# Optimization experiments

Hardware: AMD Instinct MI355X
Metric: run time of the kernel (lower is better)

Reference implementation:

```python
import jax, jax.numpy as jnp
import numpy as np

N = 100000   # nodes per node type
E = 1000000  # edges per edge type
C = 128      # channels
H = 4        # num_heads
D = C // H   # head_dim


def setup_inputs() -> dict:
    key = jax.random.key(0)
    ks = jax.random.split(key, 16)
    return {
        "x_A": jax.random.normal(ks[0], (N, C), jnp.float32),
        "x_B": jax.random.normal(ks[1], (N, C), jnp.float32),
        "Wq": jax.random.normal(ks[2], (C, C), jnp.float32) * 0.05,
        "bq": jax.random.normal(ks[3], (C,), jnp.float32) * 0.05,
        "Wk": jax.random.normal(ks[4], (C, C), jnp.float32) * 0.05,
        "bk": jax.random.normal(ks[5], (C,), jnp.float32) * 0.05,
        "Wv": jax.random.normal(ks[6], (C, C), jnp.float32) * 0.05,
        "bv": jax.random.normal(ks[7], (C,), jnp.float32) * 0.05,
        "gamma": jnp.ones((C,), jnp.float32),
        "beta": jnp.zeros((C,), jnp.float32),
        "bias_AB": jax.random.normal(ks[8], (1,), jnp.float32),
        "bias_BA": jax.random.normal(ks[9], (1,), jnp.float32),
        "sb_AB": jax.random.normal(ks[10], (E,), jnp.float32),
        "sb_BA": jax.random.normal(ks[11], (E,), jnp.float32),
        "edge_index_AB": jax.random.randint(ks[12], (2, E), 0, N, jnp.int32),
        "edge_index_BA": jax.random.randint(ks[13], (2, E), 0, N, jnp.int32),
    }


def _edge_attention(x_src, x_dst, src, dst, sb, etype_bias, Wq, bq, Wk, bk, Wv, bv):
    """Per-edge-type attention: gather -> score -> dst-segment softmax -> scatter-add."""
    n_dst = x_dst.shape[0]
    Q = (x_dst @ Wq.T + bq).reshape(n_dst, H, D)
    K = (x_src @ Wk.T + bk).reshape(-1, H, D)
    V = (x_src @ Wv.T + bv).reshape(-1, H, D)
    # [E, H] per-edge scores
    scores = jnp.einsum('ehd,ehd->eh', Q[dst], K[src]) / np.float32(np.sqrt(D))
    scores = scores + sb[:, None] + etype_bias  # spatial bias + edge-type bias
    # segment softmax over edges grouped by dst node (numerically stable)
    m = jax.ops.segment_max(scores, dst, num_segments=n_dst)
    ex = jnp.exp(scores - m[dst])
    denom = jax.ops.segment_sum(ex, dst, num_segments=n_dst)
    w = ex / denom[dst]  # [E, H]
    msg = (V[src] * w[:, :, None]).reshape(-1, C)  # [E, C]
    return jax.ops.segment_sum(msg, dst, num_segments=n_dst)  # index_add_


def _layernorm(x, gamma, beta, eps=1e-5):
    mu = x.mean(-1, keepdims=True)
    var = ((x - mu) ** 2).mean(-1, keepdims=True)
    return (x - mu) / jnp.sqrt(var + eps) * gamma + beta


def _forward(x_A, x_B, Wq, bq, Wk, bk, Wv, bv, gamma, beta,
             bias_AB, bias_BA, sb_AB, sb_BA, edge_index_AB, edge_index_BA):
    src_ab, dst_ab = edge_index_AB[0], edge_index_AB[1]  # A -> B
    src_ba, dst_ba = edge_index_BA[0], edge_index_BA[1]  # B -> A
    lin = (Wq, bq, Wk, bk, Wv, bv)
    out_B = _edge_attention(x_A, x_B, src_ab, dst_ab, sb_AB, bias_AB, *lin)
    out_A = _edge_attention(x_B, x_A, src_ba, dst_ba, sb_BA, bias_BA, *lin)
    # total degree = in_deg + out_deg per node type
    ones_e = jnp.ones((E,), jnp.float32)
    deg_A = (jax.ops.segment_sum(ones_e, src_ab, num_segments=N)
             + jax.ops.segment_sum(ones_e, dst_ba, num_segments=N))
    deg_B = (jax.ops.segment_sum(ones_e, dst_ab, num_segments=N)
             + jax.ops.segment_sum(ones_e, src_ba, num_segments=N))
    out_A = out_A + deg_A[:, None]
    out_B = out_B + deg_B[:, None]
    out_A = _layernorm(out_A + x_A, gamma, beta)
    out_B = _layernorm(out_B + x_B, gamma, beta)
    return out_A, out_B


def reference(x_A, x_B, Wq, bq, Wk, bk, Wv, bv, gamma, beta,
              bias_AB, bias_BA, sb_AB, sb_BA, edge_index_AB, edge_index_BA):
    return _forward(x_A, x_B, Wq, bq, Wk, bk, Wv, bv, gamma, beta,
                    bias_AB, bias_BA, sb_AB, sb_BA, edge_index_AB, edge_index_BA)
```

## Files before the change

### kernel.cpp

```cpp
#include <hip/hip_runtime.h>

#define CH 128
#define QSCALE (0.17677669529663687f * 1.4426950408889634f)
#define LOG2E 1.4426950408889634f
#define SCAN_BLK 1024
#define KVSTRIDE 384

typedef _Float16 f16;
typedef _Float16 f16x2 __attribute__((ext_vector_type(2)));
typedef _Float16 f16x8 __attribute__((ext_vector_type(8)));
typedef __attribute__((ext_vector_type(4))) float f32x4;

__device__ __forceinline__ unsigned pk2(float a, float b) {
    auto h = __builtin_amdgcn_cvt_pkrtz(a, b);
    return __builtin_bit_cast(unsigned, h);
}
__device__ __forceinline__ f16x2 u2h(unsigned u) { return __builtin_bit_cast(f16x2, u); }

template <int CTRL>
__device__ __forceinline__ float dpp_add(float x) {
    const int t = __builtin_amdgcn_update_dpp(0, __builtin_bit_cast(int, x), CTRL, 0xF, 0xF, false);
    return x + __builtin_bit_cast(float, t);
}
__device__ __forceinline__ float head_sum(float x) {
    x = dpp_add<0xB1>(x);
    x = dpp_add<0x4E>(x);
    x = dpp_add<0x124>(x);
    x = dpp_add<0x128>(x);
    return x;
}

__global__ __launch_bounds__(256) void wcvt(const float* __restrict__ Wq, const float* __restrict__ Wk,
                                            const float* __restrict__ Wv, unsigned short* __restrict__ out)
{
    const int i = blockIdx.x * 256 + threadIdx.x;
    if (i >= 3 * CH * CH) return;
    const float* W = (i < CH * CH) ? Wq : (i < 2 * CH * CH) ? Wk : Wv;
    const float s = (i < CH * CH) ? QSCALE : 1.f;
    f16 h = (f16)(W[i & (CH * CH - 1)] * s);
    out[i] = __builtin_bit_cast(unsigned short, h);
}

__global__ __launch_bounds__(256) void qkv_mfma(
    const float* __restrict__ xA, const float* __restrict__ xB,
    const unsigned short* __restrict__ Wb,
    const float* __restrict__ bq, const float* __restrict__ bk, const float* __restrict__ bv,
    unsigned short* __restrict__ Qb,
    unsigned char* __restrict__ KVb,
    int n)
{
    __shared__ __align__(16) char lds[40960];
    const int type = blockIdx.y;
    const float* x = type ? xB : xA;
    const int bRow = blockIdx.x * 64;
    const int tid = threadIdx.x;

    #pragma unroll
    for (int j = 0; j < 8; ++j) {
        const int flat16 = j * 256 + tid;
        const int row = flat16 >> 5;
        const int c16 = flat16 & 31;
        float4 v = make_float4(0.f, 0.f, 0.f, 0.f);
        if (bRow + row < n) v = *(const float4*)(x + (size_t)(bRow + row) * CH + c16 * 4);
        const int off = (row * 256 + c16 * 8) ^ ((row & 7) << 4);
        *(uint2*)(lds + off) = make_uint2(pk2(v.x, v.y), pk2(v.z, v.w));
    }
    __syncthreads();

    const int w = tid >> 6, l = tid & 63, lr = l & 15, lg = l >> 4;
    const int colbase = w * 32;

    f32x4 acc[3][2][4];
    #pragma unroll
    for (int p = 0; p < 3; ++p)
        #pragma unroll
        for (int ct = 0; ct < 2; ++ct)
            #pragma unroll
            for (int rt = 0; rt < 4; ++rt)
                acc[p][ct][rt] = (f32x4){0.f, 0.f, 0.f, 0.f};

    #pragma unroll
    for (int kt = 0; kt < 4; ++kt) {
        f16x8 bx[4];
        #pragma unroll
        for (int rt = 0; rt < 4; ++rt) {
            const int row = rt * 16 + lr;
            const int off = (row * 256 + kt * 64 + lg * 16) ^ ((row & 7) << 4);
            bx[rt] = *(const f16x8*)(lds + off);
        }
        #pragma unroll
        for (int p = 0; p < 3; ++p) {
            #pragma unroll
            for (int ct = 0; ct < 2; ++ct) {
                const int ocol = colbase + ct * 16 + lr;
                const f16x8 a = *(const f16x8*)(Wb + ((size_t)p << 14) + (size_t)ocol * CH + kt * 32 + lg * 8);
                #pragma unroll
                for (int rt = 0; rt < 4; ++rt)
                    acc[p][ct][rt] = __builtin_amdgcn_mfma_f32_16x16x32_f16(a, bx[rt], acc[p][ct][rt], 0, 0, 0);
            }
        }
    }

    __syncthreads();

    #pragma unroll
    for (int ct = 0; ct < 2; ++ct) {
        const int c0 = colbase + ct * 16 + lg * 4;
        float4 bbq = *(const float4*)(bq + c0);
        bbq.x *= QSCALE; bbq.y *= QSCALE; bbq.z *= QSCALE; bbq.w *= QSCALE;
        const float4 bbk = *(const float4*)(bk + c0);
        const float4 bbv = *(const float4*)(bv + c0);
        const int cbq = w * 64 + ct * 32 + lg * 8;
        const int cbk = w * 32 + ct * 16 + lg * 4;
        #pragma unroll
        for (int rt = 0; rt < 4; ++rt) {
            const int nl = rt * 16 + lr;
            const int swz = (nl & 7) << 4;
            const f32x4 aq = acc[0][ct][rt], ak = acc[1][ct][rt], av = acc[2][ct][rt];
            *(uint2*)(lds + nl * 256 + (cbq ^ swz)) =
                make_uint2(pk2(aq[0] + bbq.x, aq[1] + bbq.y), pk2(aq[2] + bbq.z, aq[3] + bbq.w));
            int kw = __builtin_amdgcn_cvt_pk_fp8_f32(ak[0] + bbk.x, ak[1] + bbk.y, 0, false);
            kw     = __builtin_amdgcn_cvt_pk_fp8_f32(ak[2] + bbk.z, ak[3] + bbk.w, kw, true);
            *(unsigned*)(lds + 16384 + nl * 128 + (cbk ^ swz)) = (unsigned)kw;
            *(uint2*)(lds + 24576 + nl * 256 + (cbq ^ swz)) =
                make_uint2(pk2(av[0] + bbv.x, av[1] + bbv.y), pk2(av[2] + bbv.z, av[3] + bbv.w));
        }
    }
    __syncthreads();

    unsigned short* Qo = Qb + (size_t)type * n * CH;
    unsigned char* KVo = KVb + (size_t)type * n * KVSTRIDE;
    #pragma unroll
    for (int j = 0; j < 4; ++j) {
        const int flat = j * 256 + tid;
        const int row = flat >> 4, c16 = flat & 15;
        const uint4 val = *(const uint4*)(lds + row * 256 + ((c16 ^ (row & 7)) << 4));
        const int node = bRow + row;
        if (node < n) *(uint4*)(Qo + (size_t)node * CH + c16 * 8) = val;
    }
    #pragma unroll
    for (int j = 0; j < 2; ++j) {
        const int flat = j * 256 + tid;
        const int row = flat >> 3, c = flat & 7;
        const uint4 val = *(const uint4*)(lds + 16384 + row * 128 + ((c ^ (row & 7)) << 4));
        const int node = bRow + row;
        if (node < n) *(uint4*)(KVo + (size_t)node * KVSTRIDE + c * 16) = val;
    }
    #pragma unroll
    for (int j = 0; j < 4; ++j) {
        const int flat = j * 256 + tid;
        const int row = flat >> 4, c16 = flat & 15;
        const uint4 val = *(const uint4*)(lds + 24576 + row * 256 + ((c16 ^ (row & 7)) << 4));
        const int node = bRow + row;
        if (node < n) *(uint4*)(KVo + (size_t)node * KVSTRIDE + 128 + c16 * 16) = val;
    }
}

__global__ __launch_bounds__(256) void deg_hist(const int* __restrict__ eiAB, const int* __restrict__ eiBA,
                                                int* __restrict__ degAB, int* __restrict__ degBA,
                                                int nE, int ebl)
{
    const int dir = blockIdx.x >= ebl;
    const int e = ((blockIdx.x - dir * ebl) * 256 + threadIdx.x) * 4;
    if (e >= nE) return;
    const int* ei = dir ? eiBA : eiAB;
    int* deg = dir ? degBA : degAB;
    if (e + 3 < nE) {
        const int4 d4 = *(const int4*)(ei + nE + e);
        atomicAdd(&deg[d4.x], 1); atomicAdd(&deg[d4.y], 1);
        atomicAdd(&deg[d4.z], 1); atomicAdd(&deg[d4.w], 1);
    } else {
        for (int j = e; j < nE; ++j) atomicAdd(&deg[ei[nE + j]], 1);
    }
}

__global__ __launch_bounds__(256) void scan_local(const int* __restrict__ degAB, const int* __restrict__ degBA,
                                                  int* __restrict__ offsAB, int* __restrict__ offsBA,
                                                  int* __restrict__ bsums, int n, int nb)
{
    __shared__ int s[256];
    const int dir = blockIdx.x >= nb;
    const int blk = blockIdx.x - dir * nb;
    const int* deg = dir ? degBA : degAB;
    int* offs = dir ? offsBA : offsAB;
    int* bs = bsums + dir * 256;

    const int t = threadIdx.x;
    const int base = blk * SCAN_BLK + t * 4;
    int v0 = 0, v1 = 0, v2 = 0, v3 = 0;
    if (base + 3 < n) {
        int4 q = *(const int4*)(deg + base);
        v0 = q.x; v1 = q.y; v2 = q.z; v3 = q.w;
    } else {
        if (base + 0 < n) v0 = deg[base + 0];
        if (base + 1 < n) v1 = deg[base + 1];
        if (base + 2 < n) v2 = deg[base + 2];
    }
    const int tsum = v0 + v1 + v2 + v3;
    s[t] = tsum;
    __syncthreads();
    for (int off = 1; off < 256; off <<= 1) {
        int add = (t >= off) ? s[t - off] : 0;
        __syncthreads();
        s[t] += add;
        __syncthreads();
    }
    const int excl = s[t] - tsum;
    if (base + 0 < n) offs[base + 0] = excl;
    if (base + 1 < n) offs[base + 1] = excl + v0;
    if (base + 2 < n) offs[base + 2] = excl + v0 + v1;
    if (base + 3 < n) offs[base + 3] = excl + v0 + v1 + v2;
    if (t == 255) bs[blk] = s[255];
}

__global__ __launch_bounds__(256) void scan_bsums(int* __restrict__ bsums, int nb)
{
    __shared__ int s[256];
    int* bs = bsums + blockIdx.x * 256;
    const int t = threadIdx.x;
    int v = (t < nb) ? bs[t] : 0;
    s[t] = v;
    __syncthreads();
    for (int off = 1; off < 256; off <<= 1) {
        int add = (t >= off) ? s[t - off] : 0;
        __syncthreads();
        s[t] += add;
        __syncthreads();
    }
    if (t < nb) bs[t] = s[t] - v;
}

__global__ __launch_bounds__(256) void add_bsums(int* __restrict__ offsAB, int* __restrict__ offsBA,
                                                 int* __restrict__ curAB, int* __restrict__ curBA,
                                                 const int* __restrict__ bsums, int n, int nbl)
{
    const int dir = blockIdx.x >= nbl;
    const int i = (blockIdx.x - dir * nbl) * 256 + threadIdx.x;
    if (i >= n) return;
    int* offs = dir ? offsBA : offsAB;
    int* cur  = dir ? curBA  : curAB;
    const int v = offs[i] + bsums[dir * 256 + (i >> 10)];
    offs[i] = v;
    cur[i] = v;
}

__global__ __launch_bounds__(256) void csr_fill(const int* __restrict__ eiAB, const int* __restrict__ eiBA,
                                                const float* __restrict__ sbAB, const float* __restrict__ sbBA,
                                                const float* __restrict__ biasAB, const float* __restrict__ biasBA,
                                                int* __restrict__ curAB, int* __restrict__ curBA,
                                                int2* __restrict__ edAB, int2* __restrict__ edBA,
                                                int nE, int ebl)
{
    const int dir = blockIdx.x >= ebl;
    const int e = ((blockIdx.x - dir * ebl) * 256 + threadIdx.x) * 4;
    if (e >= nE) return;
    const int* ei = dir ? eiBA : eiAB;
    const float* sb = dir ? sbBA : sbAB;
    const float bia = dir ? biasBA[0] : biasAB[0];
    int* cur = dir ? curBA : curAB;
    int2* ed = dir ? edBA : edAB;
    if (e + 3 < nE) {
        const int4 s4 = *(const int4*)(ei + e);
        const int4 d4 = *(const int4*)(ei + nE + e);
        const float4 b4 = *(const float4*)(sb + e);
        int p0 = atomicAdd(&cur[d4.x], 1); ed[p0] = make_int2(s4.x, __float_as_int((b4.x + bia) * LOG2E));
        int p1 = atomicAdd(&cur[d4.y], 1); ed[p1] = make_int2(s4.y, __float_as_int((b4.y + bia) * LOG2E));
        int p2 = atomicAdd(&cur[d4.z], 1); ed[p2] = make_int2(s4.z, __float_as_int((b4.z + bia) * LOG2E));
        int p3 = atomicAdd(&cur[d4.w], 1); ed[p3] = make_int2(s4.w, __float_as_int((b4.w + bia) * LOG2E));
    } else {
        for (int j = e; j < nE; ++j) {
            const int pos = atomicAdd(&cur[ei[nE + j]], 1);
            ed[pos] = make_int2(ei[j], __float_as_int((sb[j] + bia) * LOG2E));
        }
    }
}

__global__ __launch_bounds__(256) void attn_node(
    const unsigned short* __restrict__ Qb,
    const unsigned char* __restrict__ KVb,
    const float* __restrict__ xA, const float* __restrict__ xB,
    const int* __restrict__ offsAB, const int* __restrict__ offsBA,
    const int* __restrict__ degAB, const int* __restrict__ degBA,
    const int2* __restrict__ edAB, const int2* __restrict__ edBA,
    const float* __restrict__ gamma, const float* __restrict__ beta,
    float* __restrict__ out, int n, int abl)
{
    const int dir = blockIdx.x >= abl;
    const int node = (blockIdx.x - dir * abl) * 4 + (threadIdx.x >> 6);
    if (node >= n) return;
    const int l = threadIdx.x & 63;
    const int l2 = l * 2;

    const unsigned short* Q = Qb + (size_t)dir * n * CH;
    const unsigned char* KV = KVb + (size_t)(1 - dir) * n * KVSTRIDE;
    const float* x = dir ? xB : xA;
    const int* offs = dir ? offsAB : offsBA;
    const int* deg  = dir ? degAB  : degBA;
    const int2* ed  = dir ? edAB   : edBA;
    float* o = out + (size_t)dir * n * CH;

    const f16x2 qp = u2h(*(const unsigned*)(Q + (size_t)node * CH + l2));
    const float qf0 = (float)qp[0], qf1 = (float)qp[1];

    const int beg = __builtin_amdgcn_readfirstlane(offs[node]);
    const int d   = __builtin_amdgcn_readfirstlane(deg[node]);

    float m = -3.0e38f, den = 0.f;
    f16x2 a01 = (f16x2){(f16)0.f, (f16)0.f};

    auto loadE = [&](int i, float& sbf, unsigned& kc, unsigned& vc) {
        if (i < d) {
            const int2 e = ed[beg + i];
            sbf = __int_as_float(e.y);
            const unsigned b = (unsigned)e.x * (unsigned)KVSTRIDE;
            kc = *(const unsigned short*)(KV + b + l2);
            vc = *(const unsigned*)(KV + b + 128 + l2 * 2);
        } else {
            sbf = __int_as_float((int)0xFF800000u);
            kc = 0; vc = 0;
        }
    };

    auto procPair = [&](float sf0, unsigned k0, unsigned v0,
                        float sf1, unsigned k1, unsigned v1) {
        const auto kf0 = __builtin_amdgcn_cvt_pk_f32_fp8((int)k0, false);
        const auto kf1 = __builtin_amdgcn_cvt_pk_f32_fp8((int)k1, false);
        float sa = head_sum(fmaf(qf0, kf0[0], qf1 * kf0[1])) + sf0;
        float sb = head_sum(fmaf(qf0, kf1[0], qf1 * kf1[1])) + sf1;
        const float pm = fmaxf(sa, sb);
        if (!__all(pm <= m + 8.f)) {
            const float mn = fmaxf(m, pm);
            const float sc = exp2f(m - mn);
            den *= sc;
            a01 *= u2h(pk2(sc, sc));
            m = mn;
        }
        const float ea = exp2f(sa - m);
        const float eb = exp2f(sb - m);
        den += ea + eb;
        a01 += u2h(pk2(ea, ea)) * u2h(v0);
        a01 += u2h(pk2(eb, eb)) * u2h(v1);
    };

    float sA0, sA1, sA2, sA3, sB0, sB1, sB2, sB3;
    unsigned kA0, kA1, kA2, kA3, kB0, kB1, kB2, kB3;
    unsigned vA0, vA1, vA2, vA3, vB0, vB1, vB2, vB3;
    loadE(0, sA0, kA0, vA0); loadE(1, sA1, kA1, vA1);
    loadE(2, sA2, kA2, vA2); loadE(3, sA3, kA3, vA3);
    loadE(4, sB0, kB0, vB0); loadE(5, sB1, kB1, vB1);
    loadE(6, sB2, kB2, vB2); loadE(7, sB3, kB3, vB3);

    for (int i = 0; i < d; i += 8) {
        procPair(sA0, kA0, vA0, sA1, kA1, vA1);
        procPair(sA2, kA2, vA2, sA3, kA3, vA3);
        loadE(i + 8,  sA0, kA0, vA0); loadE(i + 9,  sA1, kA1, vA1);
        loadE(i + 10, sA2, kA2, vA2); loadE(i + 11, sA3, kA3, vA3);
        procPair(sB0, kB0, vB0, sB1, kB1, vB1);
        procPair(sB2, kB2, vB2, sB3, kB3, vB3);
        loadE(i + 12, sB0, kB0, vB0); loadE(i + 13, sB1, kB1, vB1);
        loadE(i + 14, sB2, kB2, vB2); loadE(i + 15, sB3, kB3, vB3);
    }

    const float inv = (den > 0.f) ? 1.f / den : 0.f;
    const float2 xv = *(const float2*)(x + (size_t)node * CH + l2);
    const float w0 = (float)a01[0] * inv + xv.x;
    const float w1 = (float)a01[1] * inv + xv.y;

    float sum = w0 + w1;
    #pragma unroll
    for (int off = 32; off; off >>= 1) sum += __shfl_xor(sum, off);
    const float mean = sum * (1.f / 128.f);
    const float c0 = w0 - mean, c1 = w1 - mean;
    float vs = c0 * c0 + c1 * c1;
    #pragma unroll
    for (int off = 32; off; off >>= 1) vs += __shfl_xor(vs, off);
    const float rstd = rsqrtf(vs * (1.f / 128.f) + 1e-5f);

    const float2 g = *(const float2*)(gamma + l2);
    const float2 bt = *(const float2*)(beta + l2);
    float2 ov;
    ov.x = c0 * rstd * g.x + bt.x;
    ov.y = c1 * rstd * g.y + bt.y;
    *(float2*)(o + (size_t)node * CH + l2) = ov;
}

extern "C" void kernel_launch(void* const* d_in, const int* in_sizes, int n_in,
                              void* d_out, int out_size, void* d_ws, size_t ws_size,
                              hipStream_t stream)
{
    const float* xA     = (const float*)d_in[0];
    const float* xB     = (const float*)d_in[1];
    const float* Wq     = (const float*)d_in[2];
    const float* bq     = (const float*)d_in[3];
    const float* Wk     = (const float*)d_in[4];
    const float* bk     = (const float*)d_in[5];
    const float* Wv     = (const float*)d_in[6];
    const float* bv     = (const float*)d_in[7];
    const float* gamma  = (const float*)d_in[8];
    const float* beta   = (const float*)d_in[9];
    const float* biasAB = (const float*)d_in[10];
    const float* biasBA = (const float*)d_in[11];
    const float* sbAB   = (const float*)d_in[12];
    const float* sbBA   = (const float*)d_in[13];
    const int*   eiAB   = (const int*)d_in[14];
    const int*   eiBA   = (const int*)d_in[15];

    const int n  = in_sizes[0] / CH;
    const int nE = in_sizes[12];
    const size_t NC = (size_t)n * CH;

    char* p = (char*)d_ws;
    auto carve = [&](size_t bytes) { char* r = p; p += (bytes + 15) & ~(size_t)15; return r; };
    unsigned short* Qb = (unsigned short*)carve(2 * NC * 2);
    unsigned char*  KVb = (unsigned char*)carve((size_t)2 * n * KVSTRIDE);
    unsigned short* Wb  = (unsigned short*)carve(3 * CH * CH * 2);
    int2* edAB  = (int2*)carve((size_t)nE * 8);
    int2* edBA  = (int2*)carve((size_t)nE * 8);
    int* offsAB = (int*)carve((size_t)n * 4);
    int* offsBA = (int*)carve((size_t)n * 4);
    int* degAB  = (int*)carve((size_t)2 * n * 4);
    int* degBA  = degAB + n;
    int* curAB  = (int*)carve((size_t)n * 4);
    int* curBA  = (int*)carve((size_t)n * 4);
    int* bsums  = (int*)carve(2 * 256 * 4);

    float* out = (float*)d_out;

    (void)hipMemsetAsync(degAB, 0, (size_t)2 * n * sizeof(int), stream);

    wcvt<<<(3 * CH * CH + 255) / 256, 256, 0, stream>>>(Wq, Wk, Wv, Wb);

    dim3 qkv_grid((n + 63) / 64, 2);
    qkv_mfma<<<qkv_grid, 256, 0, stream>>>(xA, xB, Wb, bq, bk, bv, Qb, KVb, n);

    const int ebl4 = (nE + 1023) / 1024;
    deg_hist<<<2 * ebl4, 256, 0, stream>>>(eiAB, eiBA, degAB, degBA, nE, ebl4);

    const int nb = (n + SCAN_BLK - 1) / SCAN_BLK;
    scan_local<<<2 * nb, 256, 0, stream>>>(degAB, degBA, offsAB, offsBA, bsums, n, nb);
    scan_bsums<<<2, 256, 0, stream>>>(bsums, nb);
    const int nbl = (n + 255) / 256;
    add_bsums<<<2 * nbl, 256, 0, stream>>>(offsAB, offsBA, curAB, curBA, bsums, n, nbl);

    csr_fill<<<2 * ebl4, 256, 0, stream>>>(eiAB, eiBA, sbAB, sbBA, biasAB, biasBA,
                                           curAB, curBA, edAB, edBA, nE, ebl4);

    const int abl = (n + 3) / 4;
    attn_node<<<2 * abl, 256, 0, stream>>>(Qb, KVb, xA, xB, offsAB, offsBA, degAB, degBA,
                                           edAB, edBA, gamma, beta, out, n, abl);
}
```

Baseline: 488.7 us.

## Process two nodes per wavefront with 4 channels per lane in attention

The attention kernel now maps each half-wave (32 lanes) to one destination node, so each lane handles 4 channels instead of 2. Per-head score reduction drops to three DPP steps and the LayerNorm shuffles shrink to 5 rounds. The CSR fill pre-multiplies source indices by the KV row stride to save a multiply per edge. The loop runs to the max degree of the two paired nodes, so work is wasted when their degrees differ, and edge loads are clamped instead of predicated.

```diff
diff --git a/kernel.cpp b/kernel.cpp
--- a/kernel.cpp
+++ b/kernel.cpp
@@ -22,11 +22,10 @@
     const int t = __builtin_amdgcn_update_dpp(0, __builtin_bit_cast(int, x), CTRL, 0xF, 0xF, false);
     return x + __builtin_bit_cast(float, t);
 }
-__device__ __forceinline__ float head_sum(float x) {
+__device__ __forceinline__ float head_sum8(float x) {
     x = dpp_add<0xB1>(x);
     x = dpp_add<0x4E>(x);
-    x = dpp_add<0x124>(x);
-    x = dpp_add<0x128>(x);
+    x = dpp_add<0x141>(x);
     return x;
 }
 
@@ -263,14 +262,14 @@
         const int4 s4 = *(const int4*)(ei + e);
         const int4 d4 = *(const int4*)(ei + nE + e);
         const float4 b4 = *(const float4*)(sb + e);
-        int p0 = atomicAdd(&cur[d4.x], 1); ed[p0] = make_int2(s4.x, __float_as_int((b4.x + bia) * LOG2E));
-        int p1 = atomicAdd(&cur[d4.y], 1); ed[p1] = make_int2(s4.y, __float_as_int((b4.y + bia) * LOG2E));
-        int p2 = atomicAdd(&cur[d4.z], 1); ed[p2] = make_int2(s4.z, __float_as_int((b4.z + bia) * LOG2E));
-        int p3 = atomicAdd(&cur[d4.w], 1); ed[p3] = make_int2(s4.w, __float_as_int((b4.w + bia) * LOG2E));
+        int p0 = atomicAdd(&cur[d4.x], 1); ed[p0] = make_int2(s4.x * KVSTRIDE, __float_as_int((b4.x + bia) * LOG2E));
+        int p1 = atomicAdd(&cur[d4.y], 1); ed[p1] = make_int2(s4.y * KVSTRIDE, __float_as_int((b4.y + bia) * LOG2E));
+        int p2 = atomicAdd(&cur[d4.z], 1); ed[p2] = make_int2(s4.z * KVSTRIDE, __float_as_int((b4.z + bia) * LOG2E));
+        int p3 = atomicAdd(&cur[d4.w], 1); ed[p3] = make_int2(s4.w * KVSTRIDE, __float_as_int((b4.w + bia) * LOG2E));
     } else {
         for (int j = e; j < nE; ++j) {
             const int pos = atomicAdd(&cur[ei[nE + j]], 1);
-            ed[pos] = make_int2(ei[j], __float_as_int((sb[j] + bia) * LOG2E));
+            ed[pos] = make_int2(ei[j] * KVSTRIDE, __float_as_int((sb[j] + bia) * LOG2E));
         }
     }
 }
@@ -286,10 +285,12 @@
     float* __restrict__ out, int n, int abl)
 {
     const int dir = blockIdx.x >= abl;
-    const int node = (blockIdx.x - dir * abl) * 4 + (threadIdx.x >> 6);
-    if (node >= n) return;
     const int l = threadIdx.x & 63;
-    const int l2 = l * 2;
+    const int w = threadIdx.x >> 6;
+    const int half = l >> 5;
+    const int h = l & 31;
+    const int node = (blockIdx.x - dir * abl) * 8 + w * 2 + half;
+    const int nodec = min(node, n - 1);
 
     const unsigned short* Q = Qb + (size_t)dir * n * CH;
     const unsigned char* KV = KVb + (size_t)(1 - dir) * n * KVSTRIDE;
@@ -299,89 +300,95 @@
     const int2* ed  = dir ? edAB   : edBA;
     float* o = out + (size_t)dir * n * CH;
 
-    const f16x2 qp = u2h(*(const unsigned*)(Q + (size_t)node * CH + l2));
-    const float qf0 = (float)qp[0], qf1 = (float)qp[1];
-
-    const int beg = __builtin_amdgcn_readfirstlane(offs[node]);
-    const int d   = __builtin_amdgcn_readfirstlane(deg[node]);
+    const uint2 qc = *(const uint2*)(Q + (size_t)nodec * CH + h * 4);
+    const f16x2 qh0 = u2h(qc.x), qh1 = u2h(qc.y);
+    const float q0 = (float)qh0[0], q1 = (float)qh0[1];
+    const float q2 = (float)qh1[0], q3 = (float)qh1[1];
+
+    const int beg = offs[nodec];
+    const int d = (node < n) ? deg[nodec] : 0;
+    int dmv = max(d, __shfl_xor(d, 32));
+    const int dm = __builtin_amdgcn_readfirstlane(dmv);
+
+    const unsigned kvcap = (unsigned)(n - 1) * KVSTRIDE;
+    const unsigned hk = (unsigned)h * 4u;
+    const unsigned hv = 128u + (unsigned)h * 8u;
 
     float m = -3.0e38f, den = 0.f;
     f16x2 a01 = (f16x2){(f16)0.f, (f16)0.f};
-
-    auto loadE = [&](int i, float& sbf, unsigned& kc, unsigned& vc) {
-        if (i < d) {
-            const int2 e = ed[beg + i];
-            sbf = __int_as_float(e.y);
-            const unsigned b = (unsigned)e.x * (unsigned)KVSTRIDE;
-            kc = *(const unsigned short*)(KV + b + l2);
-            vc = *(const unsigned*)(KV + b + 128 + l2 * 2);
-        } else {
-            sbf = __int_as_float((int)0xFF800000u);
-            kc = 0; vc = 0;
-        }
+    f16x2 a23 = (f16x2){(f16)0.f, (f16)0.f};
+
+    auto loadS = [&](int idx, float& sbf, unsigned& kc, uint2& vc) {
+        const int cl = max(min(idx, d - 1), 0);
+        const int2 e = ed[beg + cl];
+        sbf = (idx < d) ? __int_as_float(e.y) : __int_as_float((int)0xFF800000u);
+        const unsigned b = min((unsigned)e.x, kvcap);
+        kc = *(const unsigned*)(KV + b + hk);
+        vc = *(const uint2*)(KV + b + hv);
     };
 
-    auto procPair = [&](float sf0, unsigned k0, unsigned v0,
-                        float sf1, unsigned k1, unsigned v1) {
-        const auto kf0 = __builtin_amdgcn_cvt_pk_f32_fp8((int)k0, false);
-        const auto kf1 = __builtin_amdgcn_cvt_pk_f32_fp8((int)k1, false);
-        float sa = head_sum(fmaf(qf0, kf0[0], qf1 * kf0[1])) + sf0;
-        float sb = head_sum(fmaf(qf0, kf1[0], qf1 * kf1[1])) + sf1;
-        const float pm = fmaxf(sa, sb);
-        if (!__all(pm <= m + 8.f)) {
-            const float mn = fmaxf(m, pm);
+    auto procS = [&](float sbf, unsigned kc, uint2 vc) {
+        const auto k01 = __builtin_amdgcn_cvt_pk_f32_fp8((int)kc, false);
+        const auto k23 = __builtin_amdgcn_cvt_pk_f32_fp8((int)kc, true);
+        const float sacc = fmaf(q0, k01[0], fmaf(q1, k01[1], fmaf(q2, k23[0], q3 * k23[1])));
+        const float s = head_sum8(sacc) + sbf;
+        if (!__all(s <= m + 8.f)) {
+            const float mn = fmaxf(m, s);
             const float sc = exp2f(m - mn);
             den *= sc;
-            a01 *= u2h(pk2(sc, sc));
+            const f16x2 scp = u2h(pk2(sc, sc));
+            a01 *= scp; a23 *= scp;
             m = mn;
         }
-        const float ea = exp2f(sa - m);
-        const float eb = exp2f(sb - m);
-        den += ea + eb;
-        a01 += u2h(pk2(ea, ea)) * u2h(v0);
-        a01 += u2h(pk2(eb, eb)) * u2h(v1);
+        const float ex = exp2f(s - m);
+        den += ex;
+        const f16x2 e2 = u2h(pk2(ex, ex));
+        a01 += e2 * u2h(vc.x);
+        a23 += e2 * u2h(vc.y);
     };
 
-    float sA0, sA1, sA2, sA3, sB0, sB1, sB2, sB3;
-    unsigned kA0, kA1, kA2, kA3, kB0, kB1, kB2, kB3;
-    unsigned vA0, vA1, vA2, vA3, vB0, vB1, vB2, vB3;
-    loadE(0, sA0, kA0, vA0); loadE(1, sA1, kA1, vA1);
-    loadE(2, sA2, kA2, vA2); loadE(3, sA3, kA3, vA3);
-    loadE(4, sB0, kB0, vB0); loadE(5, sB1, kB1, vB1);
-    loadE(6, sB2, kB2, vB2); loadE(7, sB3, kB3, vB3);
-
-    for (int i = 0; i < d; i += 8) {
-        procPair(sA0, kA0, vA0, sA1, kA1, vA1);
-        procPair(sA2, kA2, vA2, sA3, kA3, vA3);
-        loadE(i + 8,  sA0, kA0, vA0); loadE(i + 9,  sA1, kA1, vA1);
-        loadE(i + 10, sA2, kA2, vA2); loadE(i + 11, sA3, kA3, vA3);
-        procPair(sB0, kB0, vB0, sB1, kB1, vB1);
-        procPair(sB2, kB2, vB2, sB3, kB3, vB3);
-        loadE(i + 12, sB0, kB0, vB0); loadE(i + 13, sB1, kB1, vB1);
-        loadE(i + 14, sB2, kB2, vB2); loadE(i + 15, sB3, kB3, vB3);
+    float s0, s1, s2, s3, s4, s5;
+    unsigned k0, k1, k2, k3, k4, k5;
+    uint2 v0, v1, v2, v3, v4, v5;
+    loadS(0, s0, k0, v0); loadS(1, s1, k1, v1); loadS(2, s2, k2, v2);
+    loadS(3, s3, k3, v3); loadS(4, s4, k4, v4); loadS(5, s5, k5, v5);
+
+    for (int j = 0; j < dm; j += 6) {
+        procS(s0, k0, v0); loadS(j + 6,  s0, k0, v0);
+        procS(s1, k1, v1); loadS(j + 7,  s1, k1, v1);
+        procS(s2, k2, v2); loadS(j + 8,  s2, k2, v2);
+        procS(s3, k3, v3); loadS(j + 9,  s3, k3, v3);
+        procS(s4, k4, v4); loadS(j + 10, s4, k4, v4);
+        procS(s5, k5, v5); loadS(j + 11, s5, k5, v5);
     }
 
     const float inv = (den > 0.f) ? 1.f / den : 0.f;
-    const float2 xv = *(const float2*)(x + (size_t)node * CH + l2);
+    const float4 xv = *(const float4*)(x + (size_t)nodec * CH + h * 4);
     const float w0 = (float)a01[0] * inv + xv.x;
     const float w1 = (float)a01[1] * inv + xv.y;
-
-    float sum = w0 + w1;
-    #pragma unroll
-    for (int off = 32; off; off >>= 1) sum += __shfl_xor(sum, off);
+    const float w2 = (float)a23[0] * inv + xv.z;
+    const float w3 = (float)a23[1] * inv + xv.w;
+
+    float sum = w0 + w1 + w2 + w3;
+    #pragma unroll
+    for (int off = 16; off; off >>= 1) sum += __shfl_xor(sum, off);
     const float mean = sum * (1.f / 128.f);
-    const float c0 = w0 - mean, c1 = w1 - mean;
-    float vs = c0 * c0 + c1 * c1;
-    #pragma unroll
-    for (int off = 32; off; off >>= 1) vs += __shfl_xor(vs, off);
+    const float c0 = w0 - mean, c1 = w1 - mean, c2 = w2 - mean, c3 = w3 - mean;
+    float vs = c0 * c0 + c1 * c1 + c2 * c2 + c3 * c3;
+    #pragma unroll
+    for (int off = 16; off; off >>= 1) vs += __shfl_xor(vs, off);
     const float rstd = rsqrtf(vs * (1.f / 128.f) + 1e-5f);
 
-    const float2 g = *(const float2*)(gamma + l2);
-    const float2 bt = *(const float2*)(beta + l2);
-    float2 ov;
-    ov.x = c0 * rstd * g.x + bt.x;
-    ov.y = c1 * rstd * g.y + bt.y;
-    *(float2*)(o + (size_t)node * CH + l2) = ov;
+    if (node < n) {
+        const float4 g = *(const float4*)(gamma + h * 4);
+        const float4 bt = *(const float4*)(beta + h * 4);
+        float4 ov;
+        ov.x = c0 * rstd * g.x + bt.x;
+        ov.y = c1 * rstd * g.y + bt.y;
+        ov.z = c2 * rstd * g.z + bt.z;
+        ov.w = c3 * rstd * g.w + bt.w;
+        *(float4*)(o + (size_t)node * CH + h * 4) = ov;
+    }
 }
 
 extern "C" void kernel_launch(void* const* d_in, const int* in_sizes, int n_in,
@@ -445,7 +452,7 @@
     csr_fill<<<2 * ebl4, 256, 0, stream>>>(eiAB, eiBA, sbAB, sbBA, biasAB, biasBA,
                                            curAB, curBA, edAB, edBA, nE, ebl4);
 
-    const int abl = (n + 3) / 4;
+    const int abl = (n + 7) / 8;
     attn_node<<<2 * abl, 256, 0, stream>>>(Qb, KVb, xA, xB, offsAB, offsBA, degAB, degBA,
                                            edAB, edBA, gamma, beta, out, n, abl);
 }
```

New measurement: 535.4 us. 9.6% more time.

## Fuse degree histogram into QKV launch, merge block-sum scan, branchless edge loads

Applied to the files above, without the earlier changes.

Merges the degree-histogram atomics into the QKV projection kernel as extra leading blocks, so the atomic-bound and MFMA-bound work can overlap in one launch. Each add_bsums block now redundantly rescans the block sums, which removes the scan_bsums launch. csr_fill stores source indices premultiplied by the KV stride. The attention edge loader becomes branchless, using clamped indices so tail loads are always valid. The cost is extra LDS scan work per add_bsums block, a larger and more varied QKV kernel, and redundant loads for padded edges.

```diff
diff --git a/kernel.cpp b/kernel.cpp
--- a/kernel.cpp
+++ b/kernel.cpp
@@ -41,18 +41,39 @@
     out[i] = __builtin_bit_cast(unsigned short, h);
 }
 
-__global__ __launch_bounds__(256) void qkv_mfma(
+__global__ __launch_bounds__(256) void qkv_hist(
     const float* __restrict__ xA, const float* __restrict__ xB,
     const unsigned short* __restrict__ Wb,
     const float* __restrict__ bq, const float* __restrict__ bk, const float* __restrict__ bv,
     unsigned short* __restrict__ Qb,
     unsigned char* __restrict__ KVb,
-    int n)
+    const int* __restrict__ eiAB, const int* __restrict__ eiBA,
+    int* __restrict__ degAB, int* __restrict__ degBA,
+    int n, int nE, int hblocks, int ebl)
 {
     __shared__ __align__(16) char lds[40960];
-    const int type = blockIdx.y;
+
+    if ((int)blockIdx.x < hblocks) {
+        const int b = blockIdx.x;
+        const int dirh = b >= ebl;
+        const int e = ((b - dirh * ebl) * 256 + threadIdx.x) * 4;
+        if (e >= nE) return;
+        const int* ei = dirh ? eiBA : eiAB;
+        int* deg = dirh ? degBA : degAB;
+        if (e + 3 < nE) {
+            const int4 d4 = *(const int4*)(ei + nE + e);
+            atomicAdd(&deg[d4.x], 1); atomicAdd(&deg[d4.y], 1);
+            atomicAdd(&deg[d4.z], 1); atomicAdd(&deg[d4.w], 1);
+        } else {
+            for (int j = e; j < nE; ++j) atomicAdd(&deg[ei[nE + j]], 1);
+        }
+        return;
+    }
+
+    const int qb = blockIdx.x - hblocks;
+    const int type = qb & 1;
     const float* x = type ? xB : xA;
-    const int bRow = blockIdx.x * 64;
+    const int bRow = (qb >> 1) * 64;
     const int tid = threadIdx.x;
 
     #pragma unroll
@@ -156,24 +177,6 @@
     }
 }
 
-__global__ __launch_bounds__(256) void deg_hist(const int* __restrict__ eiAB, const int* __restrict__ eiBA,
-                                                int* __restrict__ degAB, int* __restrict__ degBA,
-                                                int nE, int ebl)
-{
-    const int dir = blockIdx.x >= ebl;
-    const int e = ((blockIdx.x - dir * ebl) * 256 + threadIdx.x) * 4;
-    if (e >= nE) return;
-    const int* ei = dir ? eiBA : eiAB;
-    int* deg = dir ? degBA : degAB;
-    if (e + 3 < nE) {
-        const int4 d4 = *(const int4*)(ei + nE + e);
-        atomicAdd(&deg[d4.x], 1); atomicAdd(&deg[d4.y], 1);
-        atomicAdd(&deg[d4.z], 1); atomicAdd(&deg[d4.w], 1);
-    } else {
-        for (int j = e; j < nE; ++j) atomicAdd(&deg[ei[nE + j]], 1);
-    }
-}
-
 __global__ __launch_bounds__(256) void scan_local(const int* __restrict__ degAB, const int* __restrict__ degBA,
                                                   int* __restrict__ offsAB, int* __restrict__ offsBA,
                                                   int* __restrict__ bsums, int n, int nb)
@@ -213,12 +216,15 @@
     if (t == 255) bs[blk] = s[255];
 }
 
-__global__ __launch_bounds__(256) void scan_bsums(int* __restrict__ bsums, int nb)
+__global__ __launch_bounds__(256) void add_bsums(int* __restrict__ offsAB, int* __restrict__ offsBA,
+                                                 int* __restrict__ curAB, int* __restrict__ curBA,
+                                                 const int* __restrict__ bsums, int n, int nbl, int nb)
 {
     __shared__ int s[256];
-    int* bs = bsums + blockIdx.x * 256;
+    const int dir = blockIdx.x >= nbl;
+    const int blk = blockIdx.x - dir * nbl;
     const int t = threadIdx.x;
-    int v = (t < nb) ? bs[t] : 0;
+    int v = (t < nb) ? bsums[dir * 256 + t] : 0;
     s[t] = v;
     __syncthreads();
     for (int off = 1; off < 256; off <<= 1) {
@@ -227,21 +233,15 @@
         s[t] += add;
         __syncthreads();
     }
-    if (t < nb) bs[t] = s[t] - v;
-}
-
-__global__ __launch_bounds__(256) void add_bsums(int* __restrict__ offsAB, int* __restrict__ offsBA,
-                                                 int* __restrict__ curAB, int* __restrict__ curBA,
-                                                 const int* __restrict__ bsums, int n, int nbl)
-{
-    const int dir = blockIdx.x >= nbl;
-    const int i = (blockIdx.x - dir * nbl) * 256 + threadIdx.x;
+    const int i = blk * 256 + t;
     if (i >= n) return;
+    const int bi = i >> 10;
+    const int excl = (bi == 0) ? 0 : s[bi - 1];
     int* offs = dir ? offsBA : offsAB;
     int* cur  = dir ? curBA  : curAB;
-    const int v = offs[i] + bsums[dir * 256 + (i >> 10)];
-    offs[i] = v;
-    cur[i] = v;
+    const int vv = offs[i] + excl;
+    offs[i] = vv;
+    cur[i] = vv;
 }
 
 __global__ __launch_bounds__(256) void csr_fill(const int* __restrict__ eiAB, const int* __restrict__ eiBA,
@@ -263,14 +263,14 @@
         const int4 s4 = *(const int4*)(ei + e);
         const int4 d4 = *(const int4*)(ei + nE + e);
         const float4 b4 = *(const float4*)(sb + e);
-        int p0 = atomicAdd(&cur[d4.x], 1); ed[p0] = make_int2(s4.x, __float_as_int((b4.x + bia) * LOG2E));
-        int p1 = atomicAdd(&cur[d4.y], 1); ed[p1] = make_int2(s4.y, __float_as_int((b4.y + bia) * LOG2E));
-        int p2 = atomicAdd(&cur[d4.z], 1); ed[p2] = make_int2(s4.z, __float_as_int((b4.z + bia) * LOG2E));
-        int p3 = atomicAdd(&cur[d4.w], 1); ed[p3] = make_int2(s4.w, __float_as_int((b4.w + bia) * LOG2E));
+        int p0 = atomicAdd(&cur[d4.x], 1); ed[p0] = make_int2(s4.x * KVSTRIDE, __float_as_int((b4.x + bia) * LOG2E));
+        int p1 = atomicAdd(&cur[d4.y], 1); ed[p1] = make_int2(s4.y * KVSTRIDE, __float_as_int((b4.y + bia) * LOG2E));
+        int p2 = atomicAdd(&cur[d4.z], 1); ed[p2] = make_int2(s4.z * KVSTRIDE, __float_as_int((b4.z + bia) * LOG2E));
+        int p3 = atomicAdd(&cur[d4.w], 1); ed[p3] = make_int2(s4.w * KVSTRIDE, __float_as_int((b4.w + bia) * LOG2E));
     } else {
         for (int j = e; j < nE; ++j) {
             const int pos = atomicAdd(&cur[ei[nE + j]], 1);
-            ed[pos] = make_int2(ei[j], __float_as_int((sb[j] + bia) * LOG2E));
+            ed[pos] = make_int2(ei[j] * KVSTRIDE, __float_as_int((sb[j] + bia) * LOG2E));
         }
     }
 }
@@ -304,21 +304,18 @@
 
     const int beg = __builtin_amdgcn_readfirstlane(offs[node]);
     const int d   = __builtin_amdgcn_readfirstlane(deg[node]);
+    const unsigned kvcap = (unsigned)(n - 1) * KVSTRIDE;
 
     float m = -3.0e38f, den = 0.f;
     f16x2 a01 = (f16x2){(f16)0.f, (f16)0.f};
 
     auto loadE = [&](int i, float& sbf, unsigned& kc, unsigned& vc) {
-        if (i < d) {
-            const int2 e = ed[beg + i];
-            sbf = __int_as_float(e.y);
-            const unsigned b = (unsigned)e.x * (unsigned)KVSTRIDE;
-            kc = *(const unsigned short*)(KV + b + l2);
-            vc = *(const unsigned*)(KV + b + 128 + l2 * 2);
-        } else {
-            sbf = __int_as_float((int)0xFF800000u);
-            kc = 0; vc = 0;
-        }
+        const int cl = max(min(i, d - 1), 0);
+        const int2 e = ed[beg + cl];
+        sbf = (i < d) ? __int_as_float(e.y) : __int_as_float((int)0xFF800000u);
+        const unsigned b = min((unsigned)e.x, kvcap);
+        kc = *(const unsigned short*)(KV + b + l2);
+        vc = *(const unsigned*)(KV + b + 128 + l2 * 2);
     };
 
     auto procPair = [&](float sf0, unsigned k0, unsigned v0,
@@ -430,17 +427,16 @@
 
     wcvt<<<(3 * CH * CH + 255) / 256, 256, 0, stream>>>(Wq, Wk, Wv, Wb);
 
-    dim3 qkv_grid((n + 63) / 64, 2);
-    qkv_mfma<<<qkv_grid, 256, 0, stream>>>(xA, xB, Wb, bq, bk, bv, Qb, KVb, n);
-
     const int ebl4 = (nE + 1023) / 1024;
-    deg_hist<<<2 * ebl4, 256, 0, stream>>>(eiAB, eiBA, degAB, degBA, nE, ebl4);
+    const int hblocks = 2 * ebl4;
+    const int qblocks = 2 * ((n + 63) / 64);
+    qkv_hist<<<hblocks + qblocks, 256, 0, stream>>>(xA, xB, Wb, bq, bk, bv, Qb, KVb,
+                                                    eiAB, eiBA, degAB, degBA, n, nE, hblocks, ebl4);
 
     const int nb = (n + SCAN_BLK - 1) / SCAN_BLK;
     scan_local<<<2 * nb, 256, 0, stream>>>(degAB, degBA, offsAB, offsBA, bsums, n, nb);
-    scan_bsums<<<2, 256, 0, stream>>>(bsums, nb);
     const int nbl = (n + 255) / 256;
-    add_bsums<<<2 * nbl, 256, 0, stream>>>(offsAB, offsBA, curAB, curBA, bsums, n, nbl);
+    add_bsums<<<2 * nbl, 256, 0, stream>>>(offsAB, offsBA, curAB, curBA, bsums, n, nbl, nb);
 
     csr_fill<<<2 * ebl4, 256, 0, stream>>>(eiAB, eiBA, sbAB, sbBA, biasAB, biasBA,
                                            curAB, curBA, edAB, edBA, nE, ebl4);
```

Measured after the change: 503.0 us. +2.9%, slower.
